# Optimization experiments

Measured on AMD Instinct MI355X. Metric: run time of the kernel, lower is better.

## Reference

```python
import jax, jax.numpy as jnp
import numpy as np

BETA, GAMMA, ZETA = 0.66, -0.1, 1.1  # hard-concrete params
N, E, S = 20000, 640000, 256          # nodes, edges, samples (node feature dim)
D, P, PH, OUT = 2000, 500, 100, 2     # DEmRNA, pathway, pathway-hidden, out nodes


def setup_inputs() -> dict:
    key = jax.random.key(0)
    ks = jax.random.split(key, 14)
    return {
        "lnc_data": jax.random.normal(ks[0], (S, 8000), jnp.float32),
        "mi_data": jax.random.normal(ks[1], (S, 2000), jnp.float32),
        "m_data": jax.random.normal(ks[2], (S, 10000), jnp.float32),
        "src": jax.random.randint(ks[3], (E,), 0, N, dtype=jnp.int32),
        "dst": jax.random.randint(ks[4], (E,), 0, N, dtype=jnp.int32),
        "demrna_index": jax.random.randint(ks[5], (D,), 0, N, dtype=jnp.int32),
        "attn_l": jax.random.normal(ks[6], (N, 1), jnp.float32) * 0.01,
        "attn_r": jax.random.normal(ks[7], (N, 1), jnp.float32) * 0.01,
        "bias_l0": jnp.zeros((1,), jnp.float32),
        "pathway_mask": (jax.random.uniform(ks[8], (P, D)) < 0.1).astype(jnp.float32),
        "W_mp": jax.random.normal(ks[9], (P, D), jnp.float32) * (1.414 / np.sqrt(D)),
        "b_mp": jnp.zeros((P,), jnp.float32),
        "W_ph": jax.random.normal(ks[10], (PH, P), jnp.float32) * 0.05,
        "b_ph": jnp.zeros((PH,), jnp.float32),
        "W_po": jax.random.normal(ks[11], (OUT, PH), jnp.float32) * 0.1,
        "b_po": jnp.zeros((OUT,), jnp.float32),
    }


def _standardize(x):
    # torch pre_process: per-column (dim 0) mean/std, std unbiased (ddof=1)
    return (x - x.mean(axis=0)) / x.std(axis=0, ddof=1)


def reference(lnc_data, mi_data, m_data, src, dst, demrna_index,
              attn_l, attn_r, bias_l0, pathway_mask,
              W_mp, b_mp, W_ph, b_ph, W_po, b_po):
    rna = jnp.concatenate([lnc_data, mi_data, m_data], axis=1)  # [S, N]
    a_rna = _standardize(rna.T)                                  # [N, S] node feats

    # per-node attention logits (attn_l/r broadcast over sample dim)
    a1 = (a_rna * attn_l).sum(-1, keepdims=True)                 # [N, 1]
    a2 = (a_rna * attn_r).sum(-1, keepdims=True)                 # [N, 1]

    # edge attention with hard-concrete L0 gate (eval / l0_test path)
    logits = a1[src] + a2[dst] + bias_l0                         # [E, 1]
    s = jax.nn.sigmoid(logits / BETA)
    a = jnp.clip(s * (ZETA - GAMMA) + GAMMA, 0.0, 1.0)

    # custom edge-softmax: normalize by per-dst sum of gates
    z = jax.ops.segment_sum(a, dst, num_segments=N)              # [N, 1]
    a = a / z[dst]
    a = jnp.where(jnp.isnan(a), 0.0, a)                          # 0/0 -> 0

    # two rounds of u_mul_e + sum scatter aggregation
    rna1 = jax.ops.segment_sum(a * a_rna[src], dst, num_segments=N)  # [N, S]
    rna2 = jax.ops.segment_sum(a * rna1[src], dst, num_segments=N)   # [N, S]

    x = (a_rna + rna1 + rna2).T[:, demrna_index]                 # [S, D]

    # pas_net pathway branch (weight masked by pathway_mask each forward)
    h = jax.nn.relu(x @ (W_mp * pathway_mask).T + b_mp)          # [S, P]
    h = jax.nn.relu(h @ W_ph.T + b_ph)                           # [S, PH]
    return jax.nn.softmax(h @ W_po.T + b_po, axis=1)             # [S, OUT]
```

## Files before the change

### kernel.cpp

```cpp
#include <hip/hip_runtime.h>

#define NN 20000
#define EE 640000
#define SS 256
#define DD 2000
#define PP 500
#define PHH 100
#define ZSPLIT 25
#define KCH 80
#define SUB 10

typedef unsigned short ushort_t;

__device__ __forceinline__ unsigned short f2bf(float f) {
  unsigned u = __float_as_uint(f);
  unsigned r = (u + 0x7FFFu + ((u >> 16) & 1u)) >> 16;
  return (unsigned short)r;
}
__device__ __forceinline__ float lo16(unsigned u) { return __uint_as_float(u << 16); }
__device__ __forceinline__ float hi16(unsigned u) { return __uint_as_float(u & 0xFFFF0000u); }

__global__ __launch_bounds__(256) void k_meanstd(
    const float* __restrict__ lnc, const float* __restrict__ mi,
    const float* __restrict__ mdat, float* __restrict__ mean,
    float* __restrict__ invstd) {
  int s = blockIdx.x, tid = threadIdx.x;
  double sum = 0.0, ssq = 0.0;
  for (int i = tid; i < 8000; i += 256) { float v = lnc[s * 8000 + i];  sum += v; ssq += (double)v * v; }
  for (int i = tid; i < 2000; i += 256) { float v = mi[s * 2000 + i];   sum += v; ssq += (double)v * v; }
  for (int i = tid; i < 10000; i += 256){ float v = mdat[s * 10000 + i]; sum += v; ssq += (double)v * v; }
  __shared__ double sm[256], sq[256];
  sm[tid] = sum; sq[tid] = ssq; __syncthreads();
  for (int o = 128; o > 0; o >>= 1) {
    if (tid < o) { sm[tid] += sm[tid + o]; sq[tid] += sq[tid + o]; }
    __syncthreads();
  }
  if (tid == 0) {
    double mu = sm[0] / 20000.0;
    double var = (sq[0] - 20000.0 * mu * mu) / 19999.0;
    mean[s] = (float)mu;
    invstd[s] = (float)(1.0 / sqrt(var));
  }
}

__global__ __launch_bounds__(256) void k_transpose(
    const float* __restrict__ lnc, const float* __restrict__ mi,
    const float* __restrict__ mdat, const float* __restrict__ mean,
    const float* __restrict__ invstd, ushort_t* __restrict__ a_rna,
    float* __restrict__ rowsum) {
  __shared__ float tile[64][33];
  __shared__ float red[8][33];
  int nb = blockIdx.x * 32, sb = blockIdx.y * 64;
  int tx = threadIdx.x, ty = threadIdx.y;
  int n = nb + tx;
  const float* base; int w, c;
  if (n < 8000)       { base = lnc;  w = 8000;  c = n; }
  else if (n < 10000) { base = mi;   w = 2000;  c = n - 8000; }
  else                { base = mdat; w = 10000; c = n - 10000; }
  for (int r = ty; r < 64; r += 8) {
    int s = sb + r;
    tile[r][tx] = (base[(size_t)s * w + c] - mean[s]) * invstd[s];
  }
  __syncthreads();
  float ps = 0.f;
  for (int r = ty; r < 64; r += 8) ps += tile[r][tx];
  red[ty][tx] = ps;
  __syncthreads();
  if (ty == 0) {
    float t = 0.f;
    #pragma unroll
    for (int j = 0; j < 8; ++j) t += red[j][tx];
    atomicAdd(&rowsum[nb + tx], t);
  }
  ushort2* out2 = (ushort2*)a_rna;
  for (int r2 = ty; r2 < 32; r2 += 8) {
    int nn = nb + r2;
    ushort2 v;
    v.x = f2bf(tile[2 * tx][r2]);
    v.y = f2bf(tile[2 * tx + 1][r2]);
    out2[(size_t)nn * 128 + (sb >> 1) + tx] = v;
  }
}

__global__ __launch_bounds__(256) void k_a1a2f(
    const float* __restrict__ rowsum, const float* __restrict__ attnl,
    const float* __restrict__ attnr, float* __restrict__ a1, float* __restrict__ a2) {
  int n = blockIdx.x * 256 + threadIdx.x;
  if (n >= NN) return;
  float t = rowsum[n];
  a1[n] = attnl[n] * t;
  a2[n] = attnr[n] * t;
}

__global__ __launch_bounds__(256) void k_count(
    const int* __restrict__ dst, int* __restrict__ counts) {
  int e = blockIdx.x * 256 + threadIdx.x;
  if (e >= EE) return;
  atomicAdd(&counts[dst[e]], 1);
}

__global__ __launch_bounds__(1024) void k_scan(
    const int* __restrict__ counts, int* __restrict__ offsets, int* __restrict__ cursor) {
  __shared__ int sums[1024];
  int t = threadIdx.x;
  int base = t * 20;
  int local[20];
  int s = 0;
  for (int i = 0; i < 20; ++i) {
    int idx = base + i;
    int c = (idx < NN) ? counts[idx] : 0;
    local[i] = s; s += c;
  }
  sums[t] = s; __syncthreads();
  for (int d = 1; d < 1024; d <<= 1) {
    int v = (t >= d) ? sums[t - d] : 0;
    __syncthreads();
    sums[t] += v;
    __syncthreads();
  }
  int prefix = (t > 0) ? sums[t - 1] : 0;
  for (int i = 0; i < 20; ++i) {
    int idx = base + i;
    if (idx < NN) { int o = prefix + local[i]; offsets[idx] = o; cursor[idx] = o; }
  }
  if (t == 1023) offsets[NN] = sums[1023];
}

__device__ __forceinline__ float hc_gate(float l) {
  float sg = 1.0f / (1.0f + __expf(-l * 1.5151515151f));
  return fminf(fmaxf(fmaf(sg, 1.2f, -0.1f), 0.0f), 1.0f);
}

__global__ __launch_bounds__(256) void k_fill(
    const int* __restrict__ src, const int* __restrict__ dst,
    const float* __restrict__ a1, const float* __restrict__ a2,
    const float* __restrict__ bias0, int* __restrict__ cursor,
    uint2* __restrict__ csr) {
  int e = blockIdx.x * 256 + threadIdx.x;
  if (e >= EE) return;
  int d = dst[e], s = src[e];
  float a = hc_gate(a1[s] + a2[d] + bias0[0]);
  int slot = atomicAdd(&cursor[d], 1);
  uint2 rec; rec.x = (unsigned)s; rec.y = __float_as_uint(a);
  csr[slot] = rec;
}

__global__ __launch_bounds__(256) void k_znorm(
    const int* __restrict__ offs, uint2* __restrict__ csr) {
  int wave = threadIdx.x >> 6, lane = threadIdx.x & 63;
  int n = blockIdx.x * 4 + wave;
  int beg = offs[n], end = offs[n + 1];
  float z = 0.f;
  for (int i = beg + lane; i < end; i += 64) z += __uint_as_float(csr[i].y);
  for (int o = 1; o < 64; o <<= 1) z += __shfl_xor(z, o, 64);
  float inv = (z > 0.f) ? 1.0f / z : 0.0f;
  for (int i = beg + lane; i < end; i += 64) {
    uint2 rec = csr[i];
    rec.y = __float_as_uint(__uint_as_float(rec.y) * inv);
    csr[i] = rec;
  }
}

__global__ __launch_bounds__(256) void k_agg(
    const uint2* __restrict__ csr, const int* __restrict__ offs,
    const ushort_t* __restrict__ in_bf, ushort_t* __restrict__ out_bf) {
  int wave = threadIdx.x >> 6, lane = threadIdx.x & 63;
  int half = lane >> 5, sl = lane & 31;
  int n = blockIdx.x * 4 + wave;
  int beg = __builtin_amdgcn_readfirstlane(offs[n]);
  int end = __builtin_amdgcn_readfirstlane(offs[n + 1]);
  const uint4* in4 = (const uint4*)in_bf;
  float acc[8] = {0.f, 0.f, 0.f, 0.f, 0.f, 0.f, 0.f, 0.f};
  int i = beg;
  for (; i + 3 < end; i += 4) {
    uint2 rA = csr[i + half];
    uint2 rB = csr[i + 2 + half];
    uint4 vA = in4[(size_t)rA.x * 32 + sl];
    uint4 vB = in4[(size_t)rB.x * 32 + sl];
    float gA = __uint_as_float(rA.y), gB = __uint_as_float(rB.y);
    acc[0] += gA * lo16(vA.x) + gB * lo16(vB.x);
    acc[1] += gA * hi16(vA.x) + gB * hi16(vB.x);
    acc[2] += gA * lo16(vA.y) + gB * lo16(vB.y);
    acc[3] += gA * hi16(vA.y) + gB * hi16(vB.y);
    acc[4] += gA * lo16(vA.z) + gB * lo16(vB.z);
    acc[5] += gA * hi16(vA.z) + gB * hi16(vB.z);
    acc[6] += gA * lo16(vA.w) + gB * lo16(vB.w);
    acc[7] += gA * hi16(vA.w) + gB * hi16(vB.w);
  }
  for (; i + 1 < end; i += 2) {
    uint2 rA = csr[i + half];
    uint4 vA = in4[(size_t)rA.x * 32 + sl];
    float gA = __uint_as_float(rA.y);
    acc[0] += gA * lo16(vA.x); acc[1] += gA * hi16(vA.x);
    acc[2] += gA * lo16(vA.y); acc[3] += gA * hi16(vA.y);
    acc[4] += gA * lo16(vA.z); acc[5] += gA * hi16(vA.z);
    acc[6] += gA * lo16(vA.w); acc[7] += gA * hi16(vA.w);
  }
  if (i < end && half == 0) {
    uint2 rA = csr[i];
    uint4 vA = in4[(size_t)rA.x * 32 + sl];
    float gA = __uint_as_float(rA.y);
    acc[0] += gA * lo16(vA.x); acc[1] += gA * hi16(vA.x);
    acc[2] += gA * lo16(vA.y); acc[3] += gA * hi16(vA.y);
    acc[4] += gA * lo16(vA.z); acc[5] += gA * hi16(vA.z);
    acc[6] += gA * lo16(vA.w); acc[7] += gA * hi16(vA.w);
  }
  #pragma unroll
  for (int j = 0; j < 8; ++j) acc[j] += __shfl_xor(acc[j], 32, 64);
  if (half == 0) {
    uint4 w;
    w.x = (unsigned)f2bf(acc[0]) | ((unsigned)f2bf(acc[1]) << 16);
    w.y = (unsigned)f2bf(acc[2]) | ((unsigned)f2bf(acc[3]) << 16);
    w.z = (unsigned)f2bf(acc[4]) | ((unsigned)f2bf(acc[5]) << 16);
    w.w = (unsigned)f2bf(acc[6]) | ((unsigned)f2bf(acc[7]) << 16);
    ((uint4*)out_bf)[(size_t)n * 32 + sl] = w;
  }
}

__global__ __launch_bounds__(256) void k_pass2x(
    const int* __restrict__ dem, const int* __restrict__ offs,
    const uint2* __restrict__ csr, const ushort_t* __restrict__ a_rna,
    const ushort_t* __restrict__ rna1, float* __restrict__ xt) {
  int wave = threadIdx.x >> 6, lane = threadIdx.x & 63;
  int half = lane >> 5, sl = lane & 31;
  int d = blockIdx.x * 4 + wave;
  int nd = dem[d];
  const uint4* ar = (const uint4*)a_rna;
  const uint4* r1 = (const uint4*)rna1;
  int beg = __builtin_amdgcn_readfirstlane(offs[nd]);
  int end = __builtin_amdgcn_readfirstlane(offs[nd + 1]);
  float acc[8] = {0.f, 0.f, 0.f, 0.f, 0.f, 0.f, 0.f, 0.f};
  int i = beg;
  for (; i + 3 < end; i += 4) {
    uint2 rA = csr[i + half];
    uint2 rB = csr[i + 2 + half];
    uint4 vA = r1[(size_t)rA.x * 32 + sl];
    uint4 vB = r1[(size_t)rB.x * 32 + sl];
    float gA = __uint_as_float(rA.y), gB = __uint_as_float(rB.y);
    acc[0] += gA * lo16(vA.x) + gB * lo16(vB.x);
    acc[1] += gA * hi16(vA.x) + gB * hi16(vB.x);
    acc[2] += gA * lo16(vA.y) + gB * lo16(vB.y);
    acc[3] += gA * hi16(vA.y) + gB * hi16(vB.y);
    acc[4] += gA * lo16(vA.z) + gB * lo16(vB.z);
    acc[5] += gA * hi16(vA.z) + gB * hi16(vB.z);
    acc[6] += gA * lo16(vA.w) + gB * lo16(vB.w);
    acc[7] += gA * hi16(vA.w) + gB * hi16(vB.w);
  }
  for (; i + 1 < end; i += 2) {
    uint2 rA = csr[i + half];
    uint4 vA = r1[(size_t)rA.x * 32 + sl];
    float gA = __uint_as_float(rA.y);
    acc[0] += gA * lo16(vA.x); acc[1] += gA * hi16(vA.x);
    acc[2] += gA * lo16(vA.y); acc[3] += gA * hi16(vA.y);
    acc[4] += gA * lo16(vA.z); acc[5] += gA * hi16(vA.z);
    acc[6] += gA * lo16(vA.w); acc[7] += gA * hi16(vA.w);
  }
  if (i < end && half == 0) {
    uint2 rA = csr[i];
    uint4 vA = r1[(size_t)rA.x * 32 + sl];
    float gA = __uint_as_float(rA.y);
    acc[0] += gA * lo16(vA.x); acc[1] += gA * hi16(vA.x);
    acc[2] += gA * lo16(vA.y); acc[3] += gA * hi16(vA.y);
    acc[4] += gA * lo16(vA.z); acc[5] += gA * hi16(vA.z);
    acc[6] += gA * lo16(vA.w); acc[7] += gA * hi16(vA.w);
  }
  #pragma unroll
  for (int j = 0; j < 8; ++j) acc[j] += __shfl_xor(acc[j], 32, 64);
  if (half == 0) {
    uint4 va = ar[(size_t)nd * 32 + sl];
    uint4 vb = r1[(size_t)nd * 32 + sl];
    acc[0] += lo16(va.x) + lo16(vb.x); acc[1] += hi16(va.x) + hi16(vb.x);
    acc[2] += lo16(va.y) + lo16(vb.y); acc[3] += hi16(va.y) + hi16(vb.y);
    acc[4] += lo16(va.z) + lo16(vb.z); acc[5] += hi16(va.z) + hi16(vb.z);
    acc[6] += lo16(va.w) + lo16(vb.w); acc[7] += hi16(va.w) + hi16(vb.w);
    float4* xo = (float4*)&xt[(size_t)d * SS + sl * 8];
    float4 w0; w0.x = acc[0]; w0.y = acc[1]; w0.z = acc[2]; w0.w = acc[3];
    float4 w1; w1.x = acc[4]; w1.y = acc[5]; w1.z = acc[6]; w1.w = acc[7];
    xo[0] = w0; xo[1] = w1;
  }
}

__global__ __launch_bounds__(256) void k_maskw(
    const float* __restrict__ Wmp, const float* __restrict__ pmask,
    float* __restrict__ Wt) {
  __shared__ float tile[32][33];
  int p0 = blockIdx.x * 32, d0 = blockIdx.y * 32;
  int tx = threadIdx.x, ty = threadIdx.y;
  for (int r = ty; r < 32; r += 8) {
    int p = p0 + r, d = d0 + tx;
    float v = 0.f;
    if (p < PP && d < DD) v = Wmp[(size_t)p * DD + d] * pmask[(size_t)p * DD + d];
    tile[r][tx] = v;
  }
  __syncthreads();
  for (int r = ty; r < 32; r += 8) {
    int d = d0 + r, p = p0 + tx;
    if (d < DD) Wt[(size_t)d * 512 + p] = tile[tx][r];
  }
}

__global__ __launch_bounds__(256) void k_gemm1(
    const float* __restrict__ xt, const float* __restrict__ Wt,
    float* __restrict__ partial) {
  __shared__ float As[SUB][64];
  __shared__ float Ws[SUB][68];
  int tid = threadIdx.x;
  int s0 = blockIdx.x * 64, p0 = blockIdx.y * 64, d0 = blockIdx.z * KCH;
  int ts = tid & 15, tp = tid >> 4;
  float acc[4][4];
  #pragma unroll
  for (int i = 0; i < 4; ++i)
    #pragma unroll
    for (int j = 0; j < 4; ++j) acc[i][j] = 0.f;

  for (int kt = 0; kt < KCH / SUB; ++kt) {
    int dd = d0 + kt * SUB;
    #pragma unroll
    for (int i = tid; i < SUB * 64; i += 256) {
      int r = i >> 6, c = i & 63;
      As[r][c] = xt[(size_t)(dd + r) * SS + s0 + c];
    }
    #pragma unroll
    for (int i = tid; i < SUB * 64; i += 256) {
      int r = i >> 6, c = i & 63;
      Ws[r][c] = Wt[(size_t)(dd + r) * 512 + p0 + c];
    }
    __syncthreads();
    #pragma unroll
    for (int kk = 0; kk < SUB; ++kk) {
      float4 a = *(const float4*)&As[kk][ts * 4];
      float4 b = *(const float4*)&Ws[kk][tp * 4];
      acc[0][0] += a.x * b.x; acc[0][1] += a.x * b.y; acc[0][2] += a.x * b.z; acc[0][3] += a.x * b.w;
      acc[1][0] += a.y * b.x; acc[1][1] += a.y * b.y; acc[1][2] += a.y * b.z; acc[1][3] += a.y * b.w;
      acc[2][0] += a.z * b.x; acc[2][1] += a.z * b.y; acc[2][2] += a.z * b.z; acc[2][3] += a.z * b.w;
      acc[3][0] += a.w * b.x; acc[3][1] += a.w * b.y; acc[3][2] += a.w * b.z; acc[3][3] += a.w * b.w;
    }
    __syncthreads();
  }
  float* dstp = partial + (size_t)blockIdx.z * 512 * 256;
  #pragma unroll
  for (int j = 0; j < 4; ++j) {
    int p = p0 + tp * 4 + j;
    float4 w; w.x = acc[0][j]; w.y = acc[1][j]; w.z = acc[2][j]; w.w = acc[3][j];
    *(float4*)&dstp[(size_t)p * 256 + s0 + ts * 4] = w;
  }
}

__global__ __launch_bounds__(256) void k_reduce(
    const float* __restrict__ partial, const float* __restrict__ bmp,
    float* __restrict__ h1t) {
  int idx = blockIdx.x * 256 + threadIdx.x;
  if (idx >= PP * SS) return;
  float acc = bmp[idx >> 8];
  #pragma unroll
  for (int z = 0; z < ZSPLIT; ++z) acc += partial[(size_t)z * 512 * 256 + idx];
  h1t[idx] = fmaxf(acc, 0.0f);
}

__global__ __launch_bounds__(256) void k_h2(
    const float* __restrict__ h1t, const float* __restrict__ Wph,
    const float* __restrict__ bph, float* __restrict__ h2t) {
  int ph = blockIdx.x;
  int s = threadIdx.x;
  float a0 = 0.f, a1 = 0.f, a2 = 0.f, a3 = 0.f;
  for (int p = 0; p < PP; p += 4) {
    a0 += h1t[(size_t)p * SS + s]       * Wph[ph * PP + p];
    a1 += h1t[(size_t)(p + 1) * SS + s] * Wph[ph * PP + p + 1];
    a2 += h1t[(size_t)(p + 2) * SS + s] * Wph[ph * PP + p + 2];
    a3 += h1t[(size_t)(p + 3) * SS + s] * Wph[ph * PP + p + 3];
  }
  h2t[(size_t)ph * SS + s] = fmaxf(a0 + a1 + a2 + a3 + bph[ph], 0.0f);
}

__global__ __launch_bounds__(256) void k_out(
    const float* __restrict__ h2t, const float* __restrict__ Wpo,
    const float* __restrict__ bpo, float* __restrict__ out) {
  int s = threadIdx.x;
  float o0 = bpo[0], o1 = bpo[1];
  for (int ph = 0; ph < PHH; ++ph) {
    float v = h2t[(size_t)ph * SS + s];
    o0 += v * Wpo[ph];
    o1 += v * Wpo[PHH + ph];
  }
  float mx = fmaxf(o0, o1);
  float e0 = __expf(o0 - mx), e1 = __expf(o1 - mx);
  float inv = 1.0f / (e0 + e1);
  out[2 * s] = e0 * inv;
  out[2 * s + 1] = e1 * inv;
}

extern "C" void kernel_launch(void* const* d_in, const int* in_sizes, int n_in,
                              void* d_out, int out_size, void* d_ws, size_t ws_size,
                              hipStream_t stream) {
  const float* lnc   = (const float*)d_in[0];
  const float* mi    = (const float*)d_in[1];
  const float* mdat  = (const float*)d_in[2];
  const int*   src   = (const int*)d_in[3];
  const int*   dst   = (const int*)d_in[4];
  const int*   dem   = (const int*)d_in[5];
  const float* attnl = (const float*)d_in[6];
  const float* attnr = (const float*)d_in[7];
  const float* bias0 = (const float*)d_in[8];
  const float* pmask = (const float*)d_in[9];
  const float* Wmp   = (const float*)d_in[10];
  const float* bmp   = (const float*)d_in[11];
  const float* Wph   = (const float*)d_in[12];
  const float* bph   = (const float*)d_in[13];
  const float* Wpo   = (const float*)d_in[14];
  const float* bpo   = (const float*)d_in[15];
  float* out = (float*)d_out;

  char* ws = (char*)d_ws;
  size_t off = 0;
  auto alloc = [&](size_t bytes) -> char* {
    char* p = ws + off;
    off += (bytes + 255) & ~(size_t)255;
    return p;
  };
  float*    mean    = (float*)alloc(SS * 4);
  float*    invstd  = (float*)alloc(SS * 4);
  float*    a1      = (float*)alloc(NN * 4);
  float*    a2      = (float*)alloc(NN * 4);
  float*    rowsum  = (float*)alloc(NN * 4);
  int*      counts  = (int*)alloc(NN * 4);
  int*      offs    = (int*)alloc((NN + 1) * 4);
  int*      cursor  = (int*)alloc(NN * 4);
  uint2*    csr     = (uint2*)alloc((size_t)EE * 8);
  ushort_t* a_rna   = (ushort_t*)alloc((size_t)NN * SS * 2);
  ushort_t* rna1    = (ushort_t*)alloc((size_t)NN * SS * 2);
  float*    xt      = (float*)alloc((size_t)DD * SS * 4);
  float*    Wt      = (float*)alloc((size_t)DD * 512 * 4);
  float*    partial = (float*)alloc((size_t)ZSPLIT * 512 * 256 * 4);
  float*    h1t     = (float*)alloc((size_t)PP * SS * 4);
  float*    h2t     = (float*)alloc((size_t)PHH * SS * 4);

  hipMemsetAsync(rowsum, 0, (size_t)((char*)offs - (char*)rowsum), stream);

  k_meanstd<<<SS, 256, 0, stream>>>(lnc, mi, mdat, mean, invstd);
  k_transpose<<<dim3(NN / 32, SS / 64), dim3(32, 8), 0, stream>>>(lnc, mi, mdat, mean, invstd, a_rna, rowsum);
  k_a1a2f<<<(NN + 255) / 256, 256, 0, stream>>>(rowsum, attnl, attnr, a1, a2);
  k_count<<<(EE + 255) / 256, 256, 0, stream>>>(dst, counts);
  k_scan<<<1, 1024, 0, stream>>>(counts, offs, cursor);
  k_fill<<<(EE + 255) / 256, 256, 0, stream>>>(src, dst, a1, a2, bias0, cursor, csr);
  k_znorm<<<NN / 4, 256, 0, stream>>>(offs, csr);
  k_agg<<<NN / 4, 256, 0, stream>>>(csr, offs, a_rna, rna1);
  k_pass2x<<<DD / 4, 256, 0, stream>>>(dem, offs, csr, a_rna, rna1, xt);
  k_maskw<<<dim3(16, (DD + 31) / 32), dim3(32, 8), 0, stream>>>(Wmp, pmask, Wt);
  k_gemm1<<<dim3(SS / 64, 8, ZSPLIT), 256, 0, stream>>>(xt, Wt, partial);
  k_reduce<<<(PP * SS + 255) / 256, 256, 0, stream>>>(partial, bmp, h1t);
  k_h2<<<PHH, SS, 0, stream>>>(h1t, Wph, bph, h2t);
  k_out<<<1, SS, 0, stream>>>(h2t, Wpo, bpo, out);
}
```

Measured before the change: 235.4 us.

## Fuse z-normalization into aggregation, drop rowsum atomics, unroll agg, split h2

```diff
diff --git a/kernel.cpp b/kernel.cpp
--- a/kernel.cpp
+++ b/kernel.cpp
@@ -19,6 +19,11 @@
 }
 __device__ __forceinline__ float lo16(unsigned u) { return __uint_as_float(u << 16); }
 __device__ __forceinline__ float hi16(unsigned u) { return __uint_as_float(u & 0xFFFF0000u); }
+
+__global__ __launch_bounds__(256) void k_zero(uint4* __restrict__ p, int n4) {
+  int i = blockIdx.x * 256 + threadIdx.x;
+  if (i < n4) { uint4 z; z.x = 0; z.y = 0; z.z = 0; z.w = 0; p[i] = z; }
+}
 
 __global__ __launch_bounds__(256) void k_meanstd(
     const float* __restrict__ lnc, const float* __restrict__ mi,
@@ -47,7 +52,7 @@
     const float* __restrict__ lnc, const float* __restrict__ mi,
     const float* __restrict__ mdat, const float* __restrict__ mean,
     const float* __restrict__ invstd, ushort_t* __restrict__ a_rna,
-    float* __restrict__ rowsum) {
+    float* __restrict__ rowsum4) {
   __shared__ float tile[64][33];
   __shared__ float red[8][33];
   int nb = blockIdx.x * 32, sb = blockIdx.y * 64;
@@ -70,7 +75,7 @@
     float t = 0.f;
     #pragma unroll
     for (int j = 0; j < 8; ++j) t += red[j][tx];
-    atomicAdd(&rowsum[nb + tx], t);
+    rowsum4[(size_t)blockIdx.y * NN + nb + tx] = t;
   }
   ushort2* out2 = (ushort2*)a_rna;
   for (int r2 = ty; r2 < 32; r2 += 8) {
@@ -83,11 +88,11 @@
 }
 
 __global__ __launch_bounds__(256) void k_a1a2f(
-    const float* __restrict__ rowsum, const float* __restrict__ attnl,
+    const float* __restrict__ rowsum4, const float* __restrict__ attnl,
     const float* __restrict__ attnr, float* __restrict__ a1, float* __restrict__ a2) {
   int n = blockIdx.x * 256 + threadIdx.x;
   if (n >= NN) return;
-  float t = rowsum[n];
+  float t = rowsum4[n] + rowsum4[NN + n] + rowsum4[2 * NN + n] + rowsum4[3 * NN + n];
   a1[n] = attnl[n] * t;
   a2[n] = attnr[n] * t;
 }
@@ -145,39 +150,51 @@
   csr[slot] = rec;
 }
 
-__global__ __launch_bounds__(256) void k_znorm(
-    const int* __restrict__ offs, uint2* __restrict__ csr) {
-  int wave = threadIdx.x >> 6, lane = threadIdx.x & 63;
-  int n = blockIdx.x * 4 + wave;
-  int beg = offs[n], end = offs[n + 1];
-  float z = 0.f;
-  for (int i = beg + lane; i < end; i += 64) z += __uint_as_float(csr[i].y);
-  for (int o = 1; o < 64; o <<= 1) z += __shfl_xor(z, o, 64);
-  float inv = (z > 0.f) ? 1.0f / z : 0.0f;
-  for (int i = beg + lane; i < end; i += 64) {
-    uint2 rec = csr[i];
-    rec.y = __float_as_uint(__uint_as_float(rec.y) * inv);
-    csr[i] = rec;
-  }
-}
-
 __global__ __launch_bounds__(256) void k_agg(
     const uint2* __restrict__ csr, const int* __restrict__ offs,
-    const ushort_t* __restrict__ in_bf, ushort_t* __restrict__ out_bf) {
+    const ushort_t* __restrict__ in_bf, ushort_t* __restrict__ out_bf,
+    float* __restrict__ zinv) {
   int wave = threadIdx.x >> 6, lane = threadIdx.x & 63;
   int half = lane >> 5, sl = lane & 31;
   int n = blockIdx.x * 4 + wave;
   int beg = __builtin_amdgcn_readfirstlane(offs[n]);
   int end = __builtin_amdgcn_readfirstlane(offs[n + 1]);
+  float zp = 0.f;
+  for (int i = beg + lane; i < end; i += 64) zp += __uint_as_float(csr[i].y);
+  #pragma unroll
+  for (int o = 1; o < 64; o <<= 1) zp += __shfl_xor(zp, o, 64);
+  float inv = (zp > 0.f) ? 1.0f / zp : 0.0f;
+  if (lane == 0) zinv[n] = inv;
+
   const uint4* in4 = (const uint4*)in_bf;
   float acc[8] = {0.f, 0.f, 0.f, 0.f, 0.f, 0.f, 0.f, 0.f};
   int i = beg;
+  for (; i + 7 < end; i += 8) {
+    uint2 rA = csr[i + half];
+    uint2 rB = csr[i + 2 + half];
+    uint2 rC = csr[i + 4 + half];
+    uint2 rD = csr[i + 6 + half];
+    uint4 vA = in4[(size_t)rA.x * 32 + sl];
+    uint4 vB = in4[(size_t)rB.x * 32 + sl];
+    uint4 vC = in4[(size_t)rC.x * 32 + sl];
+    uint4 vD = in4[(size_t)rD.x * 32 + sl];
+    float gA = __uint_as_float(rA.y) * inv, gB = __uint_as_float(rB.y) * inv;
+    float gC = __uint_as_float(rC.y) * inv, gD = __uint_as_float(rD.y) * inv;
+    acc[0] += gA * lo16(vA.x) + gB * lo16(vB.x) + gC * lo16(vC.x) + gD * lo16(vD.x);
+    acc[1] += gA * hi16(vA.x) + gB * hi16(vB.x) + gC * hi16(vC.x) + gD * hi16(vD.x);
+    acc[2] += gA * lo16(vA.y) + gB * lo16(vB.y) + gC * lo16(vC.y) + gD * lo16(vD.y);
+    acc[3] += gA * hi16(vA.y) + gB * hi16(vB.y) + gC * hi16(vC.y) + gD * hi16(vD.y);
+    acc[4] += gA * lo16(vA.z) + gB * lo16(vB.z) + gC * lo16(vC.z) + gD * lo16(vD.z);
+    acc[5] += gA * hi16(vA.z) + gB * hi16(vB.z) + gC * hi16(vC.z) + gD * hi16(vD.z);
+    acc[6] += gA * lo16(vA.w) + gB * lo16(vB.w) + gC * lo16(vC.w) + gD * lo16(vD.w);
+    acc[7] += gA * hi16(vA.w) + gB * hi16(vB.w) + gC * hi16(vC.w) + gD * hi16(vD.w);
+  }
   for (; i + 3 < end; i += 4) {
     uint2 rA = csr[i + half];
     uint2 rB = csr[i + 2 + half];
     uint4 vA = in4[(size_t)rA.x * 32 + sl];
     uint4 vB = in4[(size_t)rB.x * 32 + sl];
-    float gA = __uint_as_float(rA.y), gB = __uint_as_float(rB.y);
+    float gA = __uint_as_float(rA.y) * inv, gB = __uint_as_float(rB.y) * inv;
     acc[0] += gA * lo16(vA.x) + gB * lo16(vB.x);
     acc[1] += gA * hi16(vA.x) + gB * hi16(vB.x);
     acc[2] += gA * lo16(vA.y) + gB * lo16(vB.y);
@@ -190,7 +207,7 @@
   for (; i + 1 < end; i += 2) {
     uint2 rA = csr[i + half];
     uint4 vA = in4[(size_t)rA.x * 32 + sl];
-    float gA = __uint_as_float(rA.y);
+    float gA = __uint_as_float(rA.y) * inv;
     acc[0] += gA * lo16(vA.x); acc[1] += gA * hi16(vA.x);
     acc[2] += gA * lo16(vA.y); acc[3] += gA * hi16(vA.y);
     acc[4] += gA * lo16(vA.z); acc[5] += gA * hi16(vA.z);
@@ -199,7 +216,7 @@
   if (i < end && half == 0) {
     uint2 rA = csr[i];
     uint4 vA = in4[(size_t)rA.x * 32 + sl];
-    float gA = __uint_as_float(rA.y);
+    float gA = __uint_as_float(rA.y) * inv;
     acc[0] += gA * lo16(vA.x); acc[1] += gA * hi16(vA.x);
     acc[2] += gA * lo16(vA.y); acc[3] += gA * hi16(vA.y);
     acc[4] += gA * lo16(vA.z); acc[5] += gA * hi16(vA.z);
@@ -220,7 +237,8 @@
 __global__ __launch_bounds__(256) void k_pass2x(
     const int* __restrict__ dem, const int* __restrict__ offs,
     const uint2* __restrict__ csr, const ushort_t* __restrict__ a_rna,
-    const ushort_t* __restrict__ rna1, float* __restrict__ xt) {
+    const ushort_t* __restrict__ rna1, const float* __restrict__ zinv,
+    float* __restrict__ xt) {
   int wave = threadIdx.x >> 6, lane = threadIdx.x & 63;
   int half = lane >> 5, sl = lane & 31;
   int d = blockIdx.x * 4 + wave;
@@ -229,6 +247,7 @@
   const uint4* r1 = (const uint4*)rna1;
   int beg = __builtin_amdgcn_readfirstlane(offs[nd]);
   int end = __builtin_amdgcn_readfirstlane(offs[nd + 1]);
+  float inv = zinv[nd];
   float acc[8] = {0.f, 0.f, 0.f, 0.f, 0.f, 0.f, 0.f, 0.f};
   int i = beg;
   for (; i + 3 < end; i += 4) {
@@ -236,7 +255,7 @@
     uint2 rB = csr[i + 2 + half];
     uint4 vA = r1[(size_t)rA.x * 32 + sl];
     uint4 vB = r1[(size_t)rB.x * 32 + sl];
-    float gA = __uint_as_float(rA.y), gB = __uint_as_float(rB.y);
+    float gA = __uint_as_float(rA.y) * inv, gB = __uint_as_float(rB.y) * inv;
     acc[0] += gA * lo16(vA.x) + gB * lo16(vB.x);
     acc[1] += gA * hi16(vA.x) + gB * hi16(vB.x);
     acc[2] += gA * lo16(vA.y) + gB * lo16(vB.y);
@@ -249,7 +268,7 @@
   for (; i + 1 < end; i += 2) {
     uint2 rA = csr[i + half];
     uint4 vA = r1[(size_t)rA.x * 32 + sl];
-    float gA = __uint_as_float(rA.y);
+    float gA = __uint_as_float(rA.y) * inv;
     acc[0] += gA * lo16(vA.x); acc[1] += gA * hi16(vA.x);
     acc[2] += gA * lo16(vA.y); acc[3] += gA * hi16(vA.y);
     acc[4] += gA * lo16(vA.z); acc[5] += gA * hi16(vA.z);
@@ -258,7 +277,7 @@
   if (i < end && half == 0) {
     uint2 rA = csr[i];
     uint4 vA = r1[(size_t)rA.x * 32 + sl];
-    float gA = __uint_as_float(rA.y);
+    float gA = __uint_as_float(rA.y) * inv;
     acc[0] += gA * lo16(vA.x); acc[1] += gA * hi16(vA.x);
     acc[2] += gA * lo16(vA.y); acc[3] += gA * hi16(vA.y);
     acc[4] += gA * lo16(vA.z); acc[5] += gA * hi16(vA.z);
@@ -357,19 +376,23 @@
   h1t[idx] = fmaxf(acc, 0.0f);
 }
 
-__global__ __launch_bounds__(256) void k_h2(
+__global__ __launch_bounds__(64) void k_h2(
     const float* __restrict__ h1t, const float* __restrict__ Wph,
     const float* __restrict__ bph, float* __restrict__ h2t) {
   int ph = blockIdx.x;
-  int s = threadIdx.x;
-  float a0 = 0.f, a1 = 0.f, a2 = 0.f, a3 = 0.f;
-  for (int p = 0; p < PP; p += 4) {
-    a0 += h1t[(size_t)p * SS + s]       * Wph[ph * PP + p];
-    a1 += h1t[(size_t)(p + 1) * SS + s] * Wph[ph * PP + p + 1];
-    a2 += h1t[(size_t)(p + 2) * SS + s] * Wph[ph * PP + p + 2];
-    a3 += h1t[(size_t)(p + 3) * SS + s] * Wph[ph * PP + p + 3];
-  }
-  h2t[(size_t)ph * SS + s] = fmaxf(a0 + a1 + a2 + a3 + bph[ph], 0.0f);
+  int s = blockIdx.y * 64 + threadIdx.x;
+  const float* w = &Wph[(size_t)ph * PP];
+  float acc[10];
+  #pragma unroll
+  for (int j = 0; j < 10; ++j) acc[j] = 0.f;
+  for (int k = 0; k < 50; ++k) {
+    int p = k * 10;
+    #pragma unroll
+    for (int j = 0; j < 10; ++j)
+      acc[j] = fmaf(h1t[(size_t)(p + j) * SS + s], w[p + j], acc[j]);
+  }
+  float t = ((acc[0] + acc[1]) + (acc[2] + acc[3])) + ((acc[4] + acc[5]) + (acc[6] + acc[7])) + (acc[8] + acc[9]);
+  h2t[(size_t)ph * SS + s] = fmaxf(t + bph[ph], 0.0f);
 }
 
 __global__ __launch_bounds__(256) void k_out(
@@ -421,7 +444,8 @@
   float*    invstd  = (float*)alloc(SS * 4);
   float*    a1      = (float*)alloc(NN * 4);
   float*    a2      = (float*)alloc(NN * 4);
-  float*    rowsum  = (float*)alloc(NN * 4);
+  float*    rowsum4 = (float*)alloc((size_t)4 * NN * 4);
+  float*    zinv    = (float*)alloc(NN * 4);
   int*      counts  = (int*)alloc(NN * 4);
   int*      offs    = (int*)alloc((NN + 1) * 4);
   int*      cursor  = (int*)alloc(NN * 4);
@@ -434,20 +458,18 @@
   float*    h1t     = (float*)alloc((size_t)PP * SS * 4);
   float*    h2t     = (float*)alloc((size_t)PHH * SS * 4);
 
-  hipMemsetAsync(rowsum, 0, (size_t)((char*)offs - (char*)rowsum), stream);
-
+  k_zero<<<(NN / 4 + 255) / 256, 256, 0, stream>>>((uint4*)counts, NN / 4);
   k_meanstd<<<SS, 256, 0, stream>>>(lnc, mi, mdat, mean, invstd);
-  k_transpose<<<dim3(NN / 32, SS / 64), dim3(32, 8), 0, stream>>>(lnc, mi, mdat, mean, invstd, a_rna, rowsum);
-  k_a1a2f<<<(NN + 255) / 256, 256, 0, stream>>>(rowsum, attnl, attnr, a1, a2);
+  k_transpose<<<dim3(NN / 32, SS / 64), dim3(32, 8), 0, stream>>>(lnc, mi, mdat, mean, invstd, a_rna, rowsum4);
+  k_a1a2f<<<(NN + 255) / 256, 256, 0, stream>>>(rowsum4, attnl, attnr, a1, a2);
   k_count<<<(EE + 255) / 256, 256, 0, stream>>>(dst, counts);
   k_scan<<<1, 1024, 0, stream>>>(counts, offs, cursor);
   k_fill<<<(EE + 255) / 256, 256, 0, stream>>>(src, dst, a1, a2, bias0, cursor, csr);
-  k_znorm<<<NN / 4, 256, 0, stream>>>(offs, csr);
-  k_agg<<<NN / 4, 256, 0, stream>>>(csr, offs, a_rna, rna1);
-  k_pass2x<<<DD / 4, 256, 0, stream>>>(dem, offs, csr, a_rna, rna1, xt);
+  k_agg<<<NN / 4, 256, 0, stream>>>(csr, offs, a_rna, rna1, zinv);
+  k_pass2x<<<DD / 4, 256, 0, stream>>>(dem, offs, csr, a_rna, rna1, zinv, xt);
   k_maskw<<<dim3(16, (DD + 31) / 32), dim3(32, 8), 0, stream>>>(Wmp, pmask, Wt);
   k_gemm1<<<dim3(SS / 64, 8, ZSPLIT), 256, 0, stream>>>(xt, Wt, partial);
   k_reduce<<<(PP * SS + 255) / 256, 256, 0, stream>>>(partial, bmp, h1t);
-  k_h2<<<PHH, SS, 0, stream>>>(h1t, Wph, bph, h2t);
+  k_h2<<<dim3(PHH, SS / 64), 64, 0, stream>>>(h1t, Wph, bph, h2t);
   k_out<<<1, SS, 0, stream>>>(h2t, Wpo, bpo, out);
 }
```

New measurement: 226.1 us. 3.9% less time.
